# Kernel tuning notes

Hardware: AMD Instinct MI355X
Metric: run time of the kernel (lower is better)

The kernel has to match this reference:

```python
import jax, jax.numpy as jnp
import numpy as np


def _lstm_layer(x_seq, w_ih, w_hh, b_ih, b_hh):
    # x_seq: [T, in], PyTorch gate order i, f, g, o
    H = w_hh.shape[1]
    h0 = jnp.zeros((H,), x_seq.dtype)

    def step(carry, x_t):
        h, c = carry
        gates = x_t @ w_ih.T + h @ w_hh.T + b_ih + b_hh  # [4H]
        i, f, g, o = jnp.split(gates, 4)
        i = jax.nn.sigmoid(i)
        f = jax.nn.sigmoid(f)
        g = jnp.tanh(g)
        o = jax.nn.sigmoid(o)
        c = f * c + i * g
        h = o * jnp.tanh(c)
        return (h, c), h

    _, hs = jax.lax.scan(step, (h0, h0), x_seq)
    return hs  # [T, H]


def setup_inputs() -> dict:
    key = jax.random.key(0)
    ks = jax.random.split(key, 12)
    B, T, n, H = 8, 128, 32, 128
    s = 1.0 / np.sqrt(H)

    def u(k, shape):
        return jax.random.uniform(k, shape, jnp.float32, -s, s)

    return {
        "x": jax.random.normal(ks[0], (B, T, n, n), jnp.float32),
        "w_ih0": u(ks[1], (4 * H, 1)),
        "w_hh0": u(ks[2], (4 * H, H)),
        "b_ih0": u(ks[3], (4 * H,)),
        "b_hh0": u(ks[4], (4 * H,)),
        "w_ih1": u(ks[5], (4 * H, H)),
        "w_hh1": u(ks[6], (4 * H, H)),
        "b_ih1": u(ks[7], (4 * H,)),
        "b_hh1": u(ks[8], (4 * H,)),
        "w_out": u(ks[9], (1, H)),
        "b_out": u(ks[10], (1,)),
    }


def reference(x, w_ih0, w_hh0, b_ih0, b_hh0, w_ih1, w_hh1, b_ih1, b_hh1, w_out, b_out):
    # x: [B, T, n, n]
    def rnn_forward(xi):  # xi: [T, n, n] -> out [T, 1]
        u = jnp.trace(xi, axis1=-2, axis2=-1)[:, None]  # [T, 1]
        h1 = _lstm_layer(u, w_ih0, w_hh0, b_ih0, b_hh0)
        h2 = _lstm_layer(h1, w_ih1, w_hh1, b_ih1, b_hh1)
        return h2 @ w_out.T + b_out  # [T, 1]

    jac = jax.vmap(jax.jacrev(rnn_forward))(x)  # [B, T, 1, T, n, n]
    d = jnp.diagonal(jac, axis1=1, axis2=3)      # [B, 1, n, n, T]
    # mirror torch: [:, 0] then transpose(2,3).transpose(1,2) -> [B, T, n, n]
    return jnp.transpose(d[:, 0], (0, 3, 1, 2))
```

## Files before the change

### kernel.cpp

```cpp
#include <hip/hip_runtime.h>
#include <math.h>

#define H    128
#define TT   128
#define CH   8

#define OFF_H1V   0
#define OFF_PARTS 262144
#define OFF_CNT   1441792

typedef __attribute__((ext_vector_type(2))) float f2;

__device__ __forceinline__ float rcpf(float x) { return __builtin_amdgcn_rcpf(x); }
__device__ __forceinline__ float sigf(float x)       { return rcpf(1.0f + __expf(-x)); }
__device__ __forceinline__ float tanhf_fast(float x) { return 1.0f - 2.0f * rcpf(1.0f + __expf(2.0f * x)); }

__device__ __forceinline__ float quad_sum(float v) {
    int t = __builtin_amdgcn_update_dpp(0, __float_as_int(v), 0xB1, 0xF, 0xF, true);
    v += __int_as_float(t);
    t = __builtin_amdgcn_update_dpp(0, __float_as_int(v), 0x4E, 0xF, 0xF, true);
    v += __int_as_float(t);
    return v;
}

__device__ __forceinline__ void wait_ge(int* ptr, int val) {
    while (__hip_atomic_load(ptr, __ATOMIC_RELAXED, __HIP_MEMORY_SCOPE_AGENT) < val)
        __builtin_amdgcn_s_sleep(1);
    (void)__hip_atomic_load(ptr, __ATOMIC_ACQUIRE, __HIP_MEMORY_SCOPE_AGENT);
}

#define BARRIER_LGKM() do { \
    asm volatile("s_waitcnt lgkmcnt(0)" ::: "memory"); \
    __builtin_amdgcn_s_barrier(); \
    asm volatile("" ::: "memory"); \
} while (0)

#define BARRIER_ALL() do { \
    asm volatile("s_waitcnt vmcnt(0) lgkmcnt(0)" ::: "memory"); \
    __builtin_amdgcn_s_barrier(); \
    asm volatile("" ::: "memory"); \
} while (0)

#define DECLW4(nm, src) \
    float4 _t_##nm = (src); \
    f2 nm##_a = {_t_##nm.x, _t_##nm.y}; \
    f2 nm##_b = {_t_##nm.z, _t_##nm.w}; \
    asm volatile("" : "+v"(nm##_a), "+v"(nm##_b));

#define LOADW_ALL(W) \
    const float4* wpa_ = (const float4*)((W) + (size_t)(rg)       * H + p * 32); \
    const float4* wpb_ = (const float4*)((W) + (size_t)(rg + 128) * H + p * 32); \
    const float4* wpc_ = (const float4*)((W) + (size_t)(rg + 256) * H + p * 32); \
    const float4* wpd_ = (const float4*)((W) + (size_t)(rg + 384) * H + p * 32); \
    DECLW4(wa0, wpa_[0]) DECLW4(wa1, wpa_[1]) DECLW4(wa2, wpa_[2]) DECLW4(wa3, wpa_[3]) \
    DECLW4(wa4, wpa_[4]) DECLW4(wa5, wpa_[5]) DECLW4(wa6, wpa_[6]) DECLW4(wa7, wpa_[7]) \
    DECLW4(wb0, wpb_[0]) DECLW4(wb1, wpb_[1]) DECLW4(wb2, wpb_[2]) DECLW4(wb3, wpb_[3]) \
    DECLW4(wb4, wpb_[4]) DECLW4(wb5, wpb_[5]) DECLW4(wb6, wpb_[6]) DECLW4(wb7, wpb_[7]) \
    DECLW4(wc0, wpc_[0]) DECLW4(wc1, wpc_[1]) DECLW4(wc2, wpc_[2]) DECLW4(wc3, wpc_[3]) \
    DECLW4(wc4, wpc_[4]) DECLW4(wc5, wpc_[5]) DECLW4(wc6, wpc_[6]) DECLW4(wc7, wpc_[7]) \
    DECLW4(wd0, wpd_[0]) DECLW4(wd1, wpd_[1]) DECLW4(wd2, wpd_[2]) DECLW4(wd3, wpd_[3]) \
    DECLW4(wd4, wpd_[4]) DECLW4(wd5, wpd_[5]) DECLW4(wd6, wpd_[6]) DECLW4(wd7, wpd_[7])

#define PKFMA(acc, w, h) \
    asm("v_pk_fma_f32 %0, %1, %2, %0" : "+v"(acc) : "v"(w), "v"(h));

#define FMA1(nm, hA, hB, acc) PKFMA(acc, nm##_a, hA) PKFMA(acc, nm##_b, hB)

#define DOTJ(j) { \
    f2 hA_ = {hv##j.x, hv##j.y}; f2 hB_ = {hv##j.z, hv##j.w}; \
    FMA1(wa##j, hA_, hB_, q0) FMA1(wb##j, hA_, hB_, q1) \
    FMA1(wc##j, hA_, hB_, q2) FMA1(wd##j, hA_, hB_, q3) }

#define DOT_BODY(HBASE) \
    const float4* _hp4 = (const float4*)(HBASE); \
    float4 hv0=_hp4[0],hv1=_hp4[1],hv2=_hp4[2],hv3=_hp4[3], \
           hv4=_hp4[4],hv5=_hp4[5],hv6=_hp4[6],hv7=_hp4[7]; \
    f2 q0={0.f,0.f},q1={0.f,0.f},q2={0.f,0.f},q3={0.f,0.f}; \
    DOTJ(0) DOTJ(1) DOTJ(2) DOTJ(3) DOTJ(4) DOTJ(5) DOTJ(6) DOTJ(7) \
    float a0=q0.x+q0.y, a1=q1.x+q1.y, a2=q2.x+q2.y, a3=q3.x+q3.y; \
    a0 = quad_sum(a0); a1 = quad_sum(a1); a2 = quad_sum(a2); a3 = quad_sum(a3);

#define B_ROUND(cstart, clen) { \
    if (r == 0) wait_ge(cntA, (cstart) + (clen)); \
    __syncthreads(); \
    if (r < (clen) * 32) { \
        int tl = r >> 5, k4 = r & 31, s = k4 >> 3, j = k4 & 7; \
        float4 v = *(const float4*)(hsrc + (size_t)((cstart) + tl) * 256 + k4 * 4); \
        *(float4*)&hb[(tl * 4 + s) * 36 + j * 4] = v; \
    } \
    __syncthreads(); \
    _Pragma("unroll") \
    for (int tl = 0; tl < (clen); tl++) { \
        DOT_BODY(hb + (tl * 4 + p) * 36) \
        float sel = (p == 0) ? a0 : (p == 1) ? a1 : (p == 2) ? a2 : a3; \
        pbase[(size_t)((cstart) + tl) * 1024 + r] = sel; \
    } \
    BARRIER_ALL(); \
    if (r == 0) \
        __hip_atomic_store(myCnt, (cstart) + (clen), __ATOMIC_RELEASE, __HIP_MEMORY_SCOPE_AGENT); }

#define C_REDUCE(pbuf, plen) { \
    const int w_ = r >> 6, l_ = r & 63; \
    if (w_ < (plen)) { \
        float v_ = gbuf[pbuf][w_][l_] + gbuf[pbuf][w_][l_ + 64]; \
        v_ = quad_sum(v_); \
        v_ += __shfl_xor(v_, 4, 64);  v_ += __shfl_xor(v_, 8, 64); \
        v_ += __shfl_xor(v_, 16, 64); v_ += __shfl_xor(v_, 32, 64); \
        if (l_ == 0) scr[w_] = v_; \
    } }

#define C_SCATTER(pstart, plen) \
    if (r < (plen) * 32) { \
        const int tl_ = r >> 5, d_ = r & 31; \
        outp[(size_t)(b * TT + (pstart) + tl_) * 1024 + d_ * 33] = scr[tl_]; \
    }

#define C_ROUND(cstart, clen, cbuf, pstart, plen, pbuf, HASPREV) { \
    if (r == 448) wait_ge(cntB1, (cstart) + (clen)); \
    if (r == 449) wait_ge(cntB2, (cstart) + (clen)); \
    if (HASPREV) { C_REDUCE(pbuf, plen) } \
    __syncthreads(); \
    if (HASPREV) { C_SCATTER(pstart, plen) } \
    float4 zf[CH], af[CH]; \
    _Pragma("unroll") \
    for (int tl = 0; tl < (clen); tl++) { \
        zf[tl] = *(const float4*)(parts + (size_t)((cstart) + tl) * 1024 + rg * 4); \
        af[tl] = *(const float4*)(parts + (size_t)((cstart) + tl) * 1024 + 512 + rg * 4); \
    } \
    _Pragma("unroll") \
    for (int tl = 0; tl < (clen); tl++) { \
        const int t = (cstart) + tl; \
        const float* hc = hbuf[t & 1]; \
        float* hx = hbuf[(t & 1) ^ 1]; \
        DOT_BODY(hc + p * 36) \
        float z0 = a0 + b0 + zf[tl].x; \
        float z1 = a1 + b1 + zf[tl].y; \
        float z2 = a2 + b2 + zf[tl].z; \
        float z3 = a3 + b3 + zf[tl].w; \
        float gi = sigf(z0), gf = sigf(z1), gg = tanhf_fast(z2), go = sigf(z3); \
        float di = gi * (1.f - gi) * af[tl].x, df = gf * (1.f - gf) * af[tl].y; \
        float dg = (1.f - gg * gg) * af[tl].z, dd = go * (1.f - go) * af[tl].w; \
        float dc = df * c2 + di * gg + gi * dg; \
        c2 = gf * c2 + gi * gg; \
        float th = tanhf_fast(c2); \
        if (p == wsl) hx[p * 36 + wpos] = go * th; \
        float dh2 = dd * th + go * (1.f - th * th) * dc; \
        if (p == 0) gbuf[cbuf][tl][rg] = wo * dh2; \
        BARRIER_LGKM(); \
    } }

__global__ __launch_bounds__(512)
__attribute__((amdgpu_waves_per_eu(1, 2)))
void pipe_kernel(const float* __restrict__ x,
                 const float* __restrict__ w_ih0,
                 const float* __restrict__ w_hh0,
                 const float* __restrict__ b_ih0,
                 const float* __restrict__ b_hh0,
                 const float* __restrict__ w_ih1,
                 const float* __restrict__ w_hh1,
                 const float* __restrict__ b_ih1,
                 const float* __restrict__ b_hh1,
                 const float* __restrict__ w_out,
                 float* __restrict__ ws,
                 float* __restrict__ outp) {
    const int role = blockIdx.x >> 3;
    const int b    = blockIdx.x & 7;
    const int r    = threadIdx.x;
    const int rg   = r >> 2, p = r & 3;
    const int wsl  = rg >> 5, wpos = rg & 31;

    int* cntA  = (int*)ws + OFF_CNT       + b * 32;
    int* cntB1 = (int*)ws + OFF_CNT + 256 + b * 32;
    int* cntB2 = (int*)ws + OFF_CNT + 512 + b * 32;
    float* h1v = ws + OFF_H1V + (size_t)b * TT * 256;

    __shared__ float hbuf[2][144];
    __shared__ float u_s[TT];
    __shared__ float scr[512];
    __shared__ float hb[CH * 144];
    __shared__ float gbuf[2][CH][128];

    if (role == 0) {
        LOADW_ALL(w_hh0)
        const float b0 = b_ih0[rg]       + b_hh0[rg];
        const float b1 = b_ih0[rg + 128] + b_hh0[rg + 128];
        const float b2 = b_ih0[rg + 256] + b_hh0[rg + 256];
        const float b3 = b_ih0[rg + 384] + b_hh0[rg + 384];
        const float wi0 = w_ih0[rg], wi1 = w_ih0[rg + 128];
        const float wi2 = w_ih0[rg + 256], wi3 = w_ih0[rg + 384];
        {
            const float* xb = x + (size_t)(b * TT + (r & 127)) * 1024;
            const int pq = r >> 7;
            float u = 0.f;
#pragma unroll
            for (int i = 0; i < 8; i++) u += xb[(pq * 8 + i) * 33];
            scr[r] = u;
        }
        if (r < 144) hbuf[0][r] = 0.f;
        __syncthreads();
        if (r < TT) u_s[r] = scr[r] + scr[r + 128] + scr[r + 256] + scr[r + 384];
        __syncthreads();

        float c1 = 0.f;
        float hn_prev = 0.f, vn_prev = 0.f;
        for (int t = 0; t < TT; t++) {
            if (t > 0) {
                if (p == 0) h1v[(t - 1) * 256 + rg] = hn_prev;
                if (p == 1) h1v[(t - 1) * 256 + 128 + rg] = vn_prev;
            }
            const float u = u_s[t];
            const float* hc = hbuf[t & 1];
            float* hx = hbuf[(t & 1) ^ 1];
            DOT_BODY(hc + p * 36)
            float z0 = a0 + fmaf(wi0, u, b0);
            float z1 = a1 + fmaf(wi1, u, b1);
            float z2 = a2 + fmaf(wi2, u, b2);
            float z3 = a3 + fmaf(wi3, u, b3);
            float gi = sigf(z0), gf = sigf(z1), gg = tanhf_fast(z2), go = sigf(z3);
            float di = gi * (1.f - gi) * wi0, df = gf * (1.f - gf) * wi1;
            float dg = (1.f - gg * gg) * wi2, dd = go * (1.f - go) * wi3;
            float dc = df * c1 + di * gg + gi * dg;
            c1 = gf * c1 + gi * gg;
            float th = tanhf_fast(c1);
            float hn = go * th;
            float vn = dd * th + go * (1.f - th * th) * dc;
            if (p == wsl) hx[p * 36 + wpos] = hn;
            hn_prev = hn; vn_prev = vn;
            if (t > 0 && ((t & (CH - 1)) == 0 || t == 124)) {
                BARRIER_ALL();
                if (r == 0)
                    __hip_atomic_store(cntA, t, __ATOMIC_RELEASE, __HIP_MEMORY_SCOPE_AGENT);
            } else {
                BARRIER_LGKM();
            }
        }
        if (p == 0) h1v[(TT - 1) * 256 + rg] = hn_prev;
        if (p == 1) h1v[(TT - 1) * 256 + 128 + rg] = vn_prev;
        BARRIER_ALL();
        if (r == 0)
            __hip_atomic_store(cntA, TT, __ATOMIC_RELEASE, __HIP_MEMORY_SCOPE_AGENT);
    } else if (role == 1 || role == 2) {
        LOADW_ALL(w_ih1)
        int* myCnt = (role == 2) ? cntB2 : cntB1;
        const float* hsrc = h1v + ((role == 2) ? 128 : 0);
        float* pbase = ws + OFF_PARTS + (size_t)b * TT * 1024 + ((role == 2) ? 512 : 0);
        for (int c = 0; c < 15; c++) { B_ROUND(c * CH, CH) }
        B_ROUND(120, 4)
        B_ROUND(124, 4)
    } else {
        LOADW_ALL(w_hh1)
        const float b0 = b_ih1[rg]       + b_hh1[rg];
        const float b1 = b_ih1[rg + 128] + b_hh1[rg + 128];
        const float b2 = b_ih1[rg + 256] + b_hh1[rg + 256];
        const float b3 = b_ih1[rg + 384] + b_hh1[rg + 384];
        const float wo = w_out[rg];
        if (r < 144) hbuf[0][r] = 0.f;
        __syncthreads();
        const float* parts = ws + OFF_PARTS + (size_t)b * TT * 1024;
        float c2 = 0.f;
        C_ROUND(0, CH, 0, 0, 0, 0, 0)
        for (int c = 1; c < 15; c++) {
            C_ROUND(c * CH, CH, c & 1, (c - 1) * CH, CH, (c - 1) & 1, 1)
        }
        C_ROUND(120, 4, 1, 112, CH, 0, 1)
        C_ROUND(124, 4, 0, 120, 4, 1, 1)
        {
            C_REDUCE(0, 4)
            BARRIER_LGKM();
            C_SCATTER(124, 4)
        }
    }
}

extern "C" void kernel_launch(void* const* d_in, const int* in_sizes, int n_in,
                              void* d_out, int out_size, void* d_ws, size_t ws_size,
                              hipStream_t stream) {
    const float* x     = (const float*)d_in[0];
    const float* w_ih0 = (const float*)d_in[1];
    const float* w_hh0 = (const float*)d_in[2];
    const float* b_ih0 = (const float*)d_in[3];
    const float* b_hh0 = (const float*)d_in[4];
    const float* w_ih1 = (const float*)d_in[5];
    const float* w_hh1 = (const float*)d_in[6];
    const float* b_ih1 = (const float*)d_in[7];
    const float* b_hh1 = (const float*)d_in[8];
    const float* w_out = (const float*)d_in[9];

    float* ws = (float*)d_ws;

    hipMemsetAsync(d_out, 0, (size_t)out_size, stream);

    pipe_kernel<<<dim3(32), dim3(512), 0, stream>>>(x, w_ih0, w_hh0, b_ih0, b_hh0,
                                                    w_ih1, w_hh1, b_ih1, b_hh1, w_out,
                                                    ws, (float*)d_out);
}
```

Baseline: 218.9 us.

## Defer tangent computation off recurrence critical path and shrink pipeline tail chunks

In both the layer-0 and layer-2 recurrences, the derivative (tangent) computation for step t is moved into step t+1, after the barrier, so the serial h/c update chain between barriers is shorter. Gate values are carried in registers across steps. The final chunk of the cross-block pipeline is also split from 4 steps into 2+1+1, with extra counter publishes at steps 126 and 127, so the consumer's drain at the end is shorter. This adds more rounds and synchronisation points near the tail and increases register pressure.

```diff
diff --git a/kernel.cpp b/kernel.cpp
--- a/kernel.cpp
+++ b/kernel.cpp
@@ -115,6 +115,13 @@
         outp[(size_t)(b * TT + (pstart) + tl_) * 1024 + d_ * 33] = scr[tl_]; \
     }
 
+#define C_DH2(IDX, GI, GF, GG, GO, TH, C2O, BUF) { \
+    float di_ = (GI) * (1.f - (GI)) * af[IDX].x, df_ = (GF) * (1.f - (GF)) * af[IDX].y; \
+    float dg_ = (1.f - (GG) * (GG)) * af[IDX].z, dd_ = (GO) * (1.f - (GO)) * af[IDX].w; \
+    float dc_ = df_ * (C2O) + di_ * (GG) + (GI) * dg_; \
+    float dh2_ = dd_ * (TH) + (GO) * (1.f - (TH) * (TH)) * dc_; \
+    if (p == 0) gbuf[BUF][IDX][rg] = wo * dh2_; }
+
 #define C_ROUND(cstart, clen, cbuf, pstart, plen, pbuf, HASPREV) { \
     if (r == 448) wait_ge(cntB1, (cstart) + (clen)); \
     if (r == 449) wait_ge(cntB2, (cstart) + (clen)); \
@@ -130,6 +137,7 @@
     _Pragma("unroll") \
     for (int tl = 0; tl < (clen); tl++) { \
         const int t = (cstart) + tl; \
+        if (tl > 0) { C_DH2(tl - 1, gi_s, gf_s, gg_s, go_s, th_s, c2o_s, cbuf) } \
         const float* hc = hbuf[t & 1]; \
         float* hx = hbuf[(t & 1) ^ 1]; \
         DOT_BODY(hc + p * 36) \
@@ -138,14 +146,12 @@
         float z2 = a2 + b2 + zf[tl].z; \
         float z3 = a3 + b3 + zf[tl].w; \
         float gi = sigf(z0), gf = sigf(z1), gg = tanhf_fast(z2), go = sigf(z3); \
-        float di = gi * (1.f - gi) * af[tl].x, df = gf * (1.f - gf) * af[tl].y; \
-        float dg = (1.f - gg * gg) * af[tl].z, dd = go * (1.f - go) * af[tl].w; \
-        float dc = df * c2 + di * gg + gi * dg; \
+        float c2o = c2; \
         c2 = gf * c2 + gi * gg; \
         float th = tanhf_fast(c2); \
         if (p == wsl) hx[p * 36 + wpos] = go * th; \
-        float dh2 = dd * th + go * (1.f - th * th) * dc; \
-        if (p == 0) gbuf[cbuf][tl][rg] = wo * dh2; \
+        gi_s = gi; gf_s = gf; gg_s = gg; go_s = go; th_s = th; c2o_s = c2o; \
+        if (tl == (clen) - 1) { C_DH2(tl, gi, gf, gg, go, th, c2o, cbuf) } \
         BARRIER_LGKM(); \
     } }
 
@@ -202,11 +208,16 @@
         __syncthreads();
 
         float c1 = 0.f;
-        float hn_prev = 0.f, vn_prev = 0.f;
+        float hn_prev = 0.f;
+        float gi_s = 0.f, gf_s = 0.f, gg_s = 0.f, go_s = 0.f, th_s = 0.f, c1o_s = 0.f;
         for (int t = 0; t < TT; t++) {
             if (t > 0) {
+                float di = gi_s * (1.f - gi_s) * wi0, df = gf_s * (1.f - gf_s) * wi1;
+                float dg = (1.f - gg_s * gg_s) * wi2, dd = go_s * (1.f - go_s) * wi3;
+                float dc = df * c1o_s + di * gg_s + gi_s * dg;
+                float vn = dd * th_s + go_s * (1.f - th_s * th_s) * dc;
                 if (p == 0) h1v[(t - 1) * 256 + rg] = hn_prev;
-                if (p == 1) h1v[(t - 1) * 256 + 128 + rg] = vn_prev;
+                if (p == 1) h1v[(t - 1) * 256 + 128 + rg] = vn;
             }
             const float u = u_s[t];
             const float* hc = hbuf[t & 1];
@@ -217,16 +228,14 @@
             float z2 = a2 + fmaf(wi2, u, b2);
             float z3 = a3 + fmaf(wi3, u, b3);
             float gi = sigf(z0), gf = sigf(z1), gg = tanhf_fast(z2), go = sigf(z3);
-            float di = gi * (1.f - gi) * wi0, df = gf * (1.f - gf) * wi1;
-            float dg = (1.f - gg * gg) * wi2, dd = go * (1.f - go) * wi3;
-            float dc = df * c1 + di * gg + gi * dg;
+            float c1o = c1;
             c1 = gf * c1 + gi * gg;
             float th = tanhf_fast(c1);
             float hn = go * th;
-            float vn = dd * th + go * (1.f - th * th) * dc;
             if (p == wsl) hx[p * 36 + wpos] = hn;
-            hn_prev = hn; vn_prev = vn;
-            if (t > 0 && ((t & (CH - 1)) == 0 || t == 124)) {
+            hn_prev = hn;
+            gi_s = gi; gf_s = gf; gg_s = gg; go_s = go; th_s = th; c1o_s = c1o;
+            if (t > 0 && ((t & (CH - 1)) == 0 || t == 124 || t == 126 || t == 127)) {
                 BARRIER_ALL();
                 if (r == 0)
                     __hip_atomic_store(cntA, t, __ATOMIC_RELEASE, __HIP_MEMORY_SCOPE_AGENT);
@@ -234,8 +243,14 @@
                 BARRIER_LGKM();
             }
         }
-        if (p == 0) h1v[(TT - 1) * 256 + rg] = hn_prev;
-        if (p == 1) h1v[(TT - 1) * 256 + 128 + rg] = vn_prev;
+        {
+            float di = gi_s * (1.f - gi_s) * wi0, df = gf_s * (1.f - gf_s) * wi1;
+            float dg = (1.f - gg_s * gg_s) * wi2, dd = go_s * (1.f - go_s) * wi3;
+            float dc = df * c1o_s + di * gg_s + gi_s * dg;
+            float vn = dd * th_s + go_s * (1.f - th_s * th_s) * dc;
+            if (p == 0) h1v[(TT - 1) * 256 + rg] = hn_prev;
+            if (p == 1) h1v[(TT - 1) * 256 + 128 + rg] = vn;
+        }
         BARRIER_ALL();
         if (r == 0)
             __hip_atomic_store(cntA, TT, __ATOMIC_RELEASE, __HIP_MEMORY_SCOPE_AGENT);
@@ -246,7 +261,9 @@
         float* pbase = ws + OFF_PARTS + (size_t)b * TT * 1024 + ((role == 2) ? 512 : 0);
         for (int c = 0; c < 15; c++) { B_ROUND(c * CH, CH) }
         B_ROUND(120, 4)
-        B_ROUND(124, 4)
+        B_ROUND(124, 2)
+        B_ROUND(126, 1)
+        B_ROUND(127, 1)
     } else {
         LOADW_ALL(w_hh1)
         const float b0 = b_ih1[rg]       + b_hh1[rg];
@@ -258,16 +275,19 @@
         __syncthreads();
         const float* parts = ws + OFF_PARTS + (size_t)b * TT * 1024;
         float c2 = 0.f;
+        float gi_s = 0.f, gf_s = 0.f, gg_s = 0.f, go_s = 0.f, th_s = 0.f, c2o_s = 0.f;
         C_ROUND(0, CH, 0, 0, 0, 0, 0)
         for (int c = 1; c < 15; c++) {
             C_ROUND(c * CH, CH, c & 1, (c - 1) * CH, CH, (c - 1) & 1, 1)
         }
         C_ROUND(120, 4, 1, 112, CH, 0, 1)
-        C_ROUND(124, 4, 0, 120, 4, 1, 1)
+        C_ROUND(124, 2, 0, 120, 4, 1, 1)
+        C_ROUND(126, 1, 1, 124, 2, 0, 1)
+        C_ROUND(127, 1, 0, 126, 1, 1, 1)
         {
-            C_REDUCE(0, 4)
+            C_REDUCE(0, 1)
             BARRIER_LGKM();
-            C_SCATTER(124, 4)
+            C_SCATTER(127, 1)
         }
     }
 }
```

Result: no change. 219.7 us (+0.4%).
